# Kernel tuning notes

Hardware: AMD Instinct MI355X
Metric: run time of the kernel (lower is better)

The kernel has to match this reference:

```python
import jax, jax.numpy as jnp
import numpy as np

DEPTH = 10


def setup_inputs() -> dict:
    key = jax.random.key(0)
    k1, k2, k3, k4 = jax.random.split(key, 4)
    B, C_in, O, D, L = 4096, 512, 1024, DEPTH, 2 ** DEPTH
    x = jax.random.normal(k1, (B, C_in), dtype=jnp.float32)
    thresholds = 6.0 * jax.random.uniform(k2, (O, D), dtype=jnp.float32) - 3.0
    ordinals = jax.random.randint(k3, (O, D), 0, C_in, dtype=jnp.int64)
    weights = jax.random.normal(k4, (O, L), dtype=jnp.float32)
    return {"x": x, "thresholds": thresholds, "ordinals": ordinals, "weights": weights}


def reference(x, thresholds, ordinals, weights):
    # x: [B, C_in]; thresholds/ordinals: [O, D]; weights: [O, 2**D]
    O, D = thresholds.shape
    # Gather the D decision features for each fern: [B, O, D]
    feats = x[:, ordinals]
    margins = feats - thresholds[None, :, :]
    # Leaf index from sign bits (bit d is MSB-first): [B, O]
    powers = (2 ** (D - 1 - jnp.arange(D))).astype(jnp.int32)
    bits = (margins > 0).astype(jnp.int32)
    leaf = jnp.sum(bits * powers, axis=-1)
    # Hinge value: minimum absolute margin along the path: [B, O]
    min_margin = jnp.min(jnp.abs(margins), axis=-1)
    # Select leaf weight per (batch, fern): w[o, leaf[b, o]]
    w_sel = jnp.take_along_axis(weights[None, :, :], leaf[:, :, None], axis=2)[..., 0]
    return w_sel * min_margin  # [B, O]
```

## Files before the change

### kernel.cpp

```cpp
#include <hip/hip_runtime.h>


#define B_TOT  4096
#define CIN    512
#define O_TOT  1024
#define DEPTH  10
#define LEAVES 1024

typedef float vf4 __attribute__((ext_vector_type(4)));

__global__ __launch_bounds__(256, 4) void transpose_kernel(
    const float* __restrict__ x,
    float* __restrict__ xT)
{
    __shared__ float tile[64 * 64];
    const int t  = threadIdx.x;
    const int c0 = blockIdx.x * 64;
    const int r0 = blockIdx.y * 64;

#pragma unroll
    for (int k = 0; k < 4; ++k) {
        const int id = k * 256 + t;
        const int r  = id >> 4;
        const int c4 = id & 15;
        const vf4 v = *reinterpret_cast<const vf4*>(
            x + (size_t)(r0 + r) * CIN + c0 + (c4 << 2));
        const int c = c4 << 2;
        tile[r * 64 + ((c + 0) ^ r)] = v.x;
        tile[r * 64 + ((c + 1) ^ r)] = v.y;
        tile[r * 64 + ((c + 2) ^ r)] = v.z;
        tile[r * 64 + ((c + 3) ^ r)] = v.w;
    }
    __syncthreads();

#pragma unroll
    for (int k = 0; k < 4; ++k) {
        const int id = k * 256 + t;
        const int c  = id >> 4;
        const int j4 = id & 15;
        vf4 v;
        v.x = tile[(j4 * 4 + 0) * 64 + (c ^ (j4 * 4 + 0))];
        v.y = tile[(j4 * 4 + 1) * 64 + (c ^ (j4 * 4 + 1))];
        v.z = tile[(j4 * 4 + 2) * 64 + (c ^ (j4 * 4 + 2))];
        v.w = tile[(j4 * 4 + 3) * 64 + (c ^ (j4 * 4 + 3))];
        *reinterpret_cast<vf4*>(xT + (size_t)(c0 + c) * B_TOT + r0 + (j4 << 2)) = v;
    }
}

__global__ __launch_bounds__(256, 4) void fern_kernel(
    const float* __restrict__ xT,
    const float* __restrict__ thresholds,
    const int*   __restrict__ ordinals,
    const float* __restrict__ weights,
    float*       __restrict__ out)
{
    __shared__ float osh[64 * 64];

    const int t    = threadIdx.x;
    const int lane = t & 63;
    const int wu   = __builtin_amdgcn_readfirstlane(t >> 6);
    const int b0   = blockIdx.x * 64;
    const int o0   = blockIdx.y * 64;

#pragma unroll 2
    for (int i = 0; i < 16; ++i) {
        const int ol = wu * 16 + i;
        const int o  = o0 + ol;
        const int*   op = ordinals   + o * DEPTH;
        const float* tp = thresholds + o * DEPTH;

        int   leaf = 0;
        float mm   = 1e30f;
#pragma unroll
        for (int d = 0; d < DEPTH; ++d) {
            const int   ord = op[d];
            const float xv  = xT[(size_t)ord * B_TOT + b0 + lane];
            const float mg  = xv - tp[d];
            leaf = (leaf << 1) | (mg > 0.0f ? 1 : 0);
            mm   = fminf(mm, fabsf(mg));
        }
        const float wv = weights[(size_t)o * LEAVES + leaf];
        osh[lane * 64 + (ol ^ lane)] = wv * mm;
    }
    __syncthreads();

#pragma unroll
    for (int k = 0; k < 4; ++k) {
        const int id = k * 256 + t;
        const int rb = id >> 4;
        const int ob = (id & 15) << 2;
        vf4 v;
        v.x = osh[rb * 64 + ((ob + 0) ^ rb)];
        v.y = osh[rb * 64 + ((ob + 1) ^ rb)];
        v.z = osh[rb * 64 + ((ob + 2) ^ rb)];
        v.w = osh[rb * 64 + ((ob + 3) ^ rb)];
        __builtin_nontemporal_store(v, reinterpret_cast<vf4*>(
            out + (size_t)(b0 + rb) * O_TOT + o0 + ob));
    }
}

extern "C" void kernel_launch(void* const* d_in, const int* in_sizes, int n_in,
                              void* d_out, int out_size, void* d_ws, size_t ws_size,
                              hipStream_t stream) {
    const float* x          = (const float*)d_in[0];
    const float* thresholds = (const float*)d_in[1];
    const int*   ordinals   = (const int*)d_in[2];
    const float* weights    = (const float*)d_in[3];
    float*       out        = (float*)d_out;
    float*       xT         = (float*)d_ws;

    dim3 tg(CIN / 64, B_TOT / 64);
    transpose_kernel<<<tg, 256, 0, stream>>>(x, xT);

    dim3 fg(B_TOT / 64, O_TOT / 64);
    fern_kernel<<<fg, 256, 0, stream>>>(xT, thresholds, ordinals, weights, out);
}
```

Baseline: 93.12 us.

## Retile fern kernel to 128 batch x 16 ferns with 2 samples per lane

Each lane now handles two adjacent batch samples, loading them as float2 from the transposed input, and all ten depth loads are issued up front before the compute loop. The block tile changes from 64x64 to 128 batch by 16 ferns, and the shared-memory staging and output write are rebuilt to match. The aim is fewer, wider global loads with more memory-level parallelism per thread and better amortisation of the ordinal and threshold reads. In exchange, output stores now cover only 16 contiguous floats (64 bytes) per row segment instead of 64, and register pressure per thread goes up.

```diff
diff --git a/kernel.cpp b/kernel.cpp
--- a/kernel.cpp
+++ b/kernel.cpp
@@ -6,8 +6,11 @@
 #define O_TOT  1024
 #define DEPTH  10
 #define LEAVES 1024
+#define BT     128
+#define OTILE  16
 
 typedef float vf4 __attribute__((ext_vector_type(4)));
+typedef float vf2 __attribute__((ext_vector_type(2)));
 
 __global__ __launch_bounds__(256, 4) void transpose_kernel(
     const float* __restrict__ x,
@@ -54,48 +57,60 @@
     const float* __restrict__ weights,
     float*       __restrict__ out)
 {
-    __shared__ float osh[64 * 64];
+    __shared__ vf2 osh[OTILE * 64];
 
     const int t    = threadIdx.x;
     const int lane = t & 63;
     const int wu   = __builtin_amdgcn_readfirstlane(t >> 6);
-    const int b0   = blockIdx.x * 64;
-    const int o0   = blockIdx.y * 64;
+    const int b0   = blockIdx.x * BT;
+    const int o0   = blockIdx.y * OTILE;
 
-#pragma unroll 2
-    for (int i = 0; i < 16; ++i) {
-        const int ol = wu * 16 + i;
+#pragma unroll
+    for (int i = 0; i < 4; ++i) {
+        const int ol = wu * 4 + i;
         const int o  = o0 + ol;
         const int*   op = ordinals   + o * DEPTH;
         const float* tp = thresholds + o * DEPTH;
 
-        int   leaf = 0;
-        float mm   = 1e30f;
+        vf2 xv[DEPTH];
+#pragma unroll
+        for (int d = 0; d < DEPTH; ++d)
+            xv[d] = *reinterpret_cast<const vf2*>(
+                xT + (size_t)op[d] * B_TOT + b0 + 2 * lane);
+
+        int   leaf0 = 0, leaf1 = 0;
+        float mm0 = 1e30f, mm1 = 1e30f;
 #pragma unroll
         for (int d = 0; d < DEPTH; ++d) {
-            const int   ord = op[d];
-            const float xv  = xT[(size_t)ord * B_TOT + b0 + lane];
-            const float mg  = xv - tp[d];
-            leaf = (leaf << 1) | (mg > 0.0f ? 1 : 0);
-            mm   = fminf(mm, fabsf(mg));
+            const float thr = tp[d];
+            const float g0  = xv[d].x - thr;
+            const float g1  = xv[d].y - thr;
+            leaf0 = (leaf0 << 1) | (g0 > 0.0f ? 1 : 0);
+            leaf1 = (leaf1 << 1) | (g1 > 0.0f ? 1 : 0);
+            mm0   = fminf(mm0, fabsf(g0));
+            mm1   = fminf(mm1, fabsf(g1));
         }
-        const float wv = weights[(size_t)o * LEAVES + leaf];
-        osh[lane * 64 + (ol ^ lane)] = wv * mm;
+        const float* wrow = weights + (size_t)o * LEAVES;
+        vf2 r;
+        r.x = wrow[leaf0] * mm0;
+        r.y = wrow[leaf1] * mm1;
+        osh[ol * 64 + (lane ^ ol)] = r;
     }
     __syncthreads();
 
+    const float* oshf = reinterpret_cast<const float*>(osh);
 #pragma unroll
-    for (int k = 0; k < 4; ++k) {
+    for (int k = 0; k < 2; ++k) {
         const int id = k * 256 + t;
-        const int rb = id >> 4;
-        const int ob = (id & 15) << 2;
+        const int r  = id >> 2;
+        const int q  = (id & 3) << 2;
         vf4 v;
-        v.x = osh[rb * 64 + ((ob + 0) ^ rb)];
-        v.y = osh[rb * 64 + ((ob + 1) ^ rb)];
-        v.z = osh[rb * 64 + ((ob + 2) ^ rb)];
-        v.w = osh[rb * 64 + ((ob + 3) ^ rb)];
+        v.x = oshf[((q + 0) * 64 + ((r >> 1) ^ (q + 0))) * 2 + (r & 1)];
+        v.y = oshf[((q + 1) * 64 + ((r >> 1) ^ (q + 1))) * 2 + (r & 1)];
+        v.z = oshf[((q + 2) * 64 + ((r >> 1) ^ (q + 2))) * 2 + (r & 1)];
+        v.w = oshf[((q + 3) * 64 + ((r >> 1) ^ (q + 3))) * 2 + (r & 1)];
         __builtin_nontemporal_store(v, reinterpret_cast<vf4*>(
-            out + (size_t)(b0 + rb) * O_TOT + o0 + ob));
+            out + (size_t)(b0 + r) * O_TOT + o0 + q));
     }
 }
 
@@ -112,6 +127,6 @@
     dim3 tg(CIN / 64, B_TOT / 64);
     transpose_kernel<<<tg, 256, 0, stream>>>(x, xT);
 
-    dim3 fg(B_TOT / 64, O_TOT / 64);
+    dim3 fg(B_TOT / BT, O_TOT / OTILE);
     fern_kernel<<<fg, 256, 0, stream>>>(xT, thresholds, ordinals, weights, out);
 }
```

Measured after the change: 87.40 us. 1.07x faster.
